# Kernel tuning notes

Measured on AMD Instinct MI355X. Metric: run time of the kernel, lower is better.

## Reference

```python
import jax, jax.numpy as jnp
import numpy as np

S_DIM, A_DIM, H_DIM = 256, 18, 256
E, NS, B = 5, 10, 4096  # ensemble, MC samples, batch


def setup_inputs() -> dict:
    key = jax.random.key(0)
    ks = iter(jax.random.split(key, 40))
    def kaiming(k, shape):
        return jax.random.normal(k, shape, jnp.float32) * np.float32(np.sqrt(2.0 / shape[-1]))
    inp = {
        "state": jax.random.normal(next(ks), (B, S_DIM), jnp.float32),
        "num_samples": NS,
    }
    dims = [(H_DIM, S_DIM), (H_DIM, H_DIM), (A_DIM, H_DIM)]
    for i, (o, ii) in enumerate(dims):
        inp[f"w_mu{i}"] = kaiming(next(ks), (E, o, ii))
        inp[f"w_rho{i}"] = jnp.full((E, o, ii), -3.0, jnp.float32)
        inp[f"b_mu{i}"] = jnp.zeros((E, o), jnp.float32)
        inp[f"b_rho{i}"] = jnp.full((E, o), -3.0, jnp.float32)
        inp[f"w_eps{i}"] = jax.random.normal(next(ks), (E, NS, o, ii), jnp.float32)
        inp[f"b_eps{i}"] = jax.random.normal(next(ks), (E, NS, o), jnp.float32)
    # uncertainty head: Linear(2A->H), ReLU, Linear(H->A), Softplus
    inp["uh_w1"] = kaiming(next(ks), (H_DIM, 2 * A_DIM))
    inp["uh_b1"] = jnp.zeros((H_DIM,), jnp.float32)
    inp["uh_w2"] = kaiming(next(ks), (A_DIM, H_DIM))
    inp["uh_b2"] = jnp.zeros((A_DIM,), jnp.float32)
    # risk head: Linear(3A->H), ReLU, Linear(H->1)
    inp["rh_w1"] = kaiming(next(ks), (H_DIM, 3 * A_DIM))
    inp["rh_b1"] = jnp.zeros((H_DIM,), jnp.float32)
    inp["rh_w2"] = kaiming(next(ks), (1, H_DIM))
    inp["rh_b2"] = jnp.zeros((1,), jnp.float32)
    return inp


def _kl(mu, sigma):
    # KL(N(mu, sigma) || N(0, 1)) summed over param dims -> per-ensemble [E]
    kl = -jnp.log(sigma) + (sigma ** 2 + mu ** 2) * 0.5 - 0.5
    return jnp.sum(kl, axis=tuple(range(1, mu.ndim)))


def _bayes(x, wmu, wrho, bmu, brho, weps, beps):
    # x: [E,S,B,in]; wmu: [E,out,in]; weps: [E,S,out,in]
    wsig = jax.nn.softplus(wrho)
    bsig = jax.nn.softplus(brho)
    w = wmu[:, None] + wsig[:, None] * weps        # [E,S,out,in]
    b = bmu[:, None] + bsig[:, None] * beps        # [E,S,out]
    y = jnp.einsum('esbi,esoi->esbo', x, w) + b[:, :, None, :]
    kl = _kl(wmu, wsig) + _kl(bmu, bsig)           # [E] (same for all MC samples)
    return y, kl


def reference(state, num_samples,
              w_mu0, w_rho0, b_mu0, b_rho0, w_eps0, b_eps0,
              w_mu1, w_rho1, b_mu1, b_rho1, w_eps1, b_eps1,
              w_mu2, w_rho2, b_mu2, b_rho2, w_eps2, b_eps2,
              uh_w1, uh_b1, uh_w2, uh_b2,
              rh_w1, rh_b1, rh_w2, rh_b2):
    e, ns = w_eps0.shape[0], w_eps0.shape[1]
    x = jnp.broadcast_to(state, (e, ns) + state.shape)          # [E,S,B,in]
    x, kl0 = _bayes(x, w_mu0, w_rho0, b_mu0, b_rho0, w_eps0, b_eps0)
    x = jax.nn.relu(x)  # dropout = identity (eval)
    x, kl1 = _bayes(x, w_mu1, w_rho1, b_mu1, b_rho1, w_eps1, b_eps1)
    x = jax.nn.relu(x)
    x, kl2 = _bayes(x, w_mu2, w_rho2, b_mu2, b_rho2, w_eps2, b_eps2)
    net_out = x.mean(axis=1)                                     # [E,B,A]
    q_mean = net_out.mean(axis=0)                                # [B,A]
    q_var = jnp.var(net_out, axis=0, ddof=1)                     # unbiased, as torch .var
    epistemic = q_var
    u_in = jnp.concatenate([q_mean, q_var], axis=-1)             # [B,2A]
    h = jax.nn.relu(u_in @ uh_w1.T + uh_b1)
    aleatoric = jax.nn.softplus(h @ uh_w2.T + uh_b2)             # [B,A]
    total_unc = epistemic + aleatoric
    r_in = jnp.concatenate([q_mean, epistemic, aleatoric], axis=-1)  # [B,3A]
    risk = jax.nn.relu(r_in @ rh_w1.T + rh_b1) @ rh_w2.T + rh_b2     # [B,1]
    s = 2.0 * jnp.sqrt(total_unc)
    lcb, ucb = q_mean - s, q_mean + s
    # total_kl = sum_e ns*kl_e ; divided by (E*num_samples) -> mean over ensemble
    kl_div = jnp.sum(kl0 + kl1 + kl2) / e
    return (q_mean, epistemic, aleatoric, total_unc, lcb, ucb, risk, kl_div)
```

## Files before the change

### kernel.cpp

```cpp
#include <hip/hip_runtime.h>
#include <hip/hip_bf16.h>


typedef __bf16 bf16x8 __attribute__((ext_vector_type(8)));
typedef float f32x4 __attribute__((ext_vector_type(4)));
typedef float f32x16 __attribute__((ext_vector_type(16)));
typedef unsigned short u16x4 __attribute__((ext_vector_type(4)));
typedef unsigned short u16x8 __attribute__((ext_vector_type(8)));

__device__ __forceinline__ unsigned short f2bf(float f) {
  unsigned int u = __builtin_bit_cast(unsigned int, f);
  u += 0x7fffu + ((u >> 16) & 1u);
  return (unsigned short)(u >> 16);
}

__device__ __forceinline__ float softplus_f(float x) {
  return (x > 20.f) ? x : __logf(1.f + __expf(x));
}

__device__ __forceinline__ float klterm(float m, float sg) {
  return -__logf(sg) + (sg * sg + m * m) * 0.5f - 0.5f;
}

__device__ __forceinline__ f32x16 mfma32(bf16x8 a, bf16x8 b, f32x16 c) {
  return __builtin_amdgcn_mfma_f32_32x32x16_bf16(a, b, c, 0, 0, 0);
}

template <int O>
__device__ __forceinline__ float wpanel_body(
    int p, int t, const float* __restrict__ wmu, const float* __restrict__ wrho,
    const float* __restrict__ weps, char* __restrict__ wf,
    char* __restrict__ lb) {
  int es = (O == 256) ? (p >> 3) : p;
  int osub = (O == 256) ? (p & 7) : 0;
  int e = es / 10, s = es - e * 10;
  float kl = 0.f;
  int i = (4 * t) & 255;
  int kt2 = i >> 4, byo = (i & 7) * 2, hi32 = 32 * ((i >> 3) & 1);
#pragma unroll
  for (int j = 0; j < 8; ++j) {
    int o = j * 4 + (t >> 6);
    int og = osub * 32 + o;
    float v[4];
    if (O == 256 || og < O) {
      size_t base = ((size_t)(e * O + og)) * 256 + i;
      f32x4 m4 = *(const f32x4*)(wmu + base);
      f32x4 r4 = *(const f32x4*)(wrho + base);
      f32x4 e4 = *(const f32x4*)(weps + ((size_t)((e * 10 + s) * O + og)) * 256 + i);
#pragma unroll
      for (int c = 0; c < 4; ++c) {
        float m = m4[c];
        float sg = softplus_f(r4[c]);
        v[c] = m + sg * e4[c];
        if (s == 0) kl += klterm(m, sg);
      }
    } else {
#pragma unroll
      for (int c = 0; c < 4; ++c) v[c] = 0.f;
    }
    u16x4 pk = {f2bf(v[0]), f2bf(v[1]), f2bf(v[2]), f2bf(v[3])};
    *(u16x4*)(lb + kt2 * 1024 + (o + hi32) * 16 + byo) = pk;
  }
  __syncthreads();
  char* dst = wf + (size_t)p * 16384;
#pragma unroll
  for (int j = 0; j < 4; ++j) {
    int idx = j * 256 + t;
    *(u16x8*)(dst + idx * 16) = *(const u16x8*)(lb + idx * 16);
  }
  return kl;
}

__device__ __forceinline__ void scvt_body(int gid, const float* __restrict__ s,
                                          unsigned short* __restrict__ d) {
  const f32x4* p = (const f32x4*)(s + (size_t)gid * 8);
  f32x4 x0 = p[0], x1 = p[1];
  u16x8 v = {f2bf(x0.x), f2bf(x0.y), f2bf(x0.z), f2bf(x0.w),
             f2bf(x1.x), f2bf(x1.y), f2bf(x1.z), f2bf(x1.w)};
  *(u16x8*)(d + (size_t)gid * 8) = v;
}

__global__ __launch_bounds__(256) void prep_kernel(
    const float* __restrict__ state, unsigned short* __restrict__ stateb,
    const float* __restrict__ wmu0, const float* __restrict__ wrho0,
    const float* __restrict__ weps0, char* __restrict__ W0f,
    const float* __restrict__ wmu1, const float* __restrict__ wrho1,
    const float* __restrict__ weps1, char* __restrict__ W1f,
    const float* __restrict__ wmu2, const float* __restrict__ wrho2,
    const float* __restrict__ weps2, char* __restrict__ W2f,
    const float* __restrict__ bmu0, const float* __restrict__ brho0,
    const float* __restrict__ beps0, const float* __restrict__ bmu1,
    const float* __restrict__ brho1, const float* __restrict__ beps1,
    const float* __restrict__ bmu2, const float* __restrict__ brho2,
    const float* __restrict__ beps2, float* __restrict__ bias0,
    float* __restrict__ bias1, float* __restrict__ bias2,
    float* __restrict__ partials) {
  __shared__ char lb[16384];
  int bid = blockIdx.x, t = threadIdx.x;
  float kl = 0.f;
  if (bid < 512) {
    scvt_body(bid * 256 + t, state, stateb);
  } else if (bid < 912) {
    kl = wpanel_body<256>(bid - 512, t, wmu0, wrho0, weps0, W0f, lb);
  } else if (bid < 1312) {
    kl = wpanel_body<256>(bid - 912, t, wmu1, wrho1, weps1, W1f, lb);
  } else if (bid < 1362) {
    kl = wpanel_body<18>(bid - 1312, t, wmu2, wrho2, weps2, W2f, lb);
  } else {
    int gid = (bid - 1362) * 256 + t;
    if (gid < 12800) {
      int es = gid >> 8, o = gid & 255, e = es / 10, s = es - e * 10;
      float m = bmu0[e * 256 + o];
      float sg = softplus_f(brho0[e * 256 + o]);
      bias0[gid] = m + sg * beps0[(e * 10 + s) * 256 + o];
      if (s == 0) kl = klterm(m, sg);
    } else if (gid < 25600) {
      int id = gid - 12800;
      int es = id >> 8, o = id & 255, e = es / 10, s = es - e * 10;
      float m = bmu1[e * 256 + o];
      float sg = softplus_f(brho1[e * 256 + o]);
      bias1[id] = m + sg * beps1[(e * 10 + s) * 256 + o];
      if (s == 0) kl = klterm(m, sg);
    } else if (gid < 27200) {
      int id = gid - 25600;
      int es = id >> 5, o = id & 31, e = es / 10, s = es - e * 10;
      if (o < 18) {
        float m = bmu2[e * 18 + o];
        float sg = softplus_f(brho2[e * 18 + o]);
        bias2[id] = m + sg * beps2[(e * 10 + s) * 18 + o];
        if (s == 0) kl = klterm(m, sg);
      } else {
        bias2[id] = 0.f;
      }
    }
  }
#pragma unroll
  for (int m = 32; m >= 1; m >>= 1) kl += __shfl_xor(kl, m);
  __shared__ float wsum[4];
  if ((t & 63) == 0) wsum[t >> 6] = kl;
  __syncthreads();
  if (t == 0) partials[bid] = wsum[0] + wsum[1] + wsum[2] + wsum[3];
}

__device__ __forceinline__ void mlp_layer32(const char* __restrict__ wA,
                                            const float* __restrict__ bias_es,
                                            int og, char* __restrict__ buf,
                                            int lane) {
  const char* a0p = wA + (size_t)(2 * og) * 16384;
  const char* a1p = a0p + 16384;
  const char* b0p = buf;
  const char* b1p = buf + 16384;
  int lo = lane * 16;
  f32x16 acc00, acc01, acc10, acc11;
#pragma unroll
  for (int c = 0; c < 16; ++c) {
    acc00[c] = 0.f; acc01[c] = 0.f; acc10[c] = 0.f; acc11[c] = 0.f;
  }

  bf16x8 a0c = *(const bf16x8*)(a0p + lo);
  bf16x8 a1c = *(const bf16x8*)(a1p + lo);
  bf16x8 b0c = *(const bf16x8*)(b0p + lo);
  bf16x8 b1c = *(const bf16x8*)(b1p + lo);
#pragma unroll
  for (int kp = 0; kp < 8; ++kp) {
    bf16x8 a0n = *(const bf16x8*)(a0p + (2 * kp + 1) * 1024 + lo);
    bf16x8 a1n = *(const bf16x8*)(a1p + (2 * kp + 1) * 1024 + lo);
    bf16x8 b0n = *(const bf16x8*)(b0p + (2 * kp + 1) * 1024 + lo);
    bf16x8 b1n = *(const bf16x8*)(b1p + (2 * kp + 1) * 1024 + lo);
    __builtin_amdgcn_s_setprio(1);
    acc00 = mfma32(a0c, b0c, acc00);
    acc01 = mfma32(a0c, b1c, acc01);
    acc10 = mfma32(a1c, b0c, acc10);
    acc11 = mfma32(a1c, b1c, acc11);
    __builtin_amdgcn_s_setprio(0);
    if (kp < 7) {
      a0c = *(const bf16x8*)(a0p + (2 * kp + 2) * 1024 + lo);
      a1c = *(const bf16x8*)(a1p + (2 * kp + 2) * 1024 + lo);
      b0c = *(const bf16x8*)(b0p + (2 * kp + 2) * 1024 + lo);
      b1c = *(const bf16x8*)(b1p + (2 * kp + 2) * 1024 + lo);
    }
    __builtin_amdgcn_s_setprio(1);
    acc00 = mfma32(a0n, b0n, acc00);
    acc01 = mfma32(a0n, b1n, acc01);
    acc10 = mfma32(a1n, b0n, acc10);
    acc11 = mfma32(a1n, b1n, acc11);
    __builtin_amdgcn_s_setprio(0);
  }
  __syncthreads();

  int hi = lane >> 5, bcol = lane & 31;
  auto epi = [&](const f32x16& A, int i, int j) {
    int obt = og * 64 + i * 32;
    char* fb = buf + (size_t)(j * 16) * 1024;
#pragma unroll
    for (int q = 0; q < 4; ++q) {
      int o0 = obt + 8 * q + 4 * hi;
      f32x4 bv = *(const f32x4*)(bias_es + o0);
      float v0 = fmaxf(A[4 * q + 0] + bv.x, 0.f);
      float v1 = fmaxf(A[4 * q + 1] + bv.y, 0.f);
      float v2 = fmaxf(A[4 * q + 2] + bv.z, 0.f);
      float v3 = fmaxf(A[4 * q + 3] + bv.w, 0.f);
      u16x4 pk = {f2bf(v0), f2bf(v1), f2bf(v2), f2bf(v3)};
      int kt2t = o0 >> 4;
      *(u16x4*)(fb + kt2t * 1024 + (bcol + 32 * (q & 1)) * 16 + 8 * hi) = pk;
    }
  };
  epi(acc00, 0, 0);
  epi(acc01, 0, 1);
  epi(acc10, 1, 0);
  epi(acc11, 1, 1);
  __syncthreads();
}

__global__ __launch_bounds__(256, 4) void mlp_fused(
    const unsigned short* __restrict__ stateb, const char* __restrict__ W0f,
    const char* __restrict__ W1f, const char* __restrict__ W2f,
    const float* __restrict__ bias0, const float* __restrict__ bias1,
    const float* __restrict__ bias2, float* __restrict__ y2) {
  __shared__ char buf[32768];
  int tid = threadIdx.x, w = tid >> 6, lane = tid & 63;
  int lo = lane * 16;

  int bid = blockIdx.x;
  int lin = (bid & 7) * 400 + (bid >> 3);
  int es = lin >> 6, b0 = (lin & 63) * 64;
  int og = w;

#pragma unroll
  for (int it = 0; it < 8; ++it) {
    int F = it * 4 + w, bt = F >> 4, kt2 = F & 15;
    const unsigned short* src =
        stateb + (size_t)(b0 + bt * 32 + (lane & 31)) * 256 + kt2 * 16 + (lane >> 5) * 8;
    *(u16x8*)(buf + F * 1024 + lo) = *(const u16x8*)src;
  }
  __syncthreads();

  mlp_layer32(W0f + (size_t)es * 131072, bias0 + es * 256, og, buf, lane);
  mlp_layer32(W1f + (size_t)es * 131072, bias1 + es * 256, og, buf, lane);

  if (w < 2) {
    int bt2 = w;
    f32x16 acc2;
#pragma unroll
    for (int c = 0; c < 16; ++c) acc2[c] = 0.f;
    const char* b2k = buf + (size_t)bt2 * 16384;
    const char* w2p = W2f + (size_t)es * 16384;
#pragma unroll
    for (int k = 0; k < 16; ++k) {
      bf16x8 a = *(const bf16x8*)(w2p + k * 1024 + lo);
      bf16x8 bb = *(const bf16x8*)(b2k + k * 1024 + lo);
      acc2 = mfma32(a, bb, acc2);
    }
    int hi = lane >> 5, bcol = lane & 31;
    int b_idx = b0 + bt2 * 32 + bcol;
    float* yp = y2 + ((size_t)es * 4096 + b_idx) * 20;
    float s[16];
#pragma unroll
    for (int q = 0; q < 4; ++q) {
      f32x4 bv = *(const f32x4*)(bias2 + es * 32 + 8 * q + 4 * hi);
      s[4 * q + 0] = acc2[4 * q + 0] + bv.x;
      s[4 * q + 1] = acc2[4 * q + 1] + bv.y;
      s[4 * q + 2] = acc2[4 * q + 2] + bv.z;
      s[4 * q + 3] = acc2[4 * q + 3] + bv.w;
    }
    if (hi == 0) {
      f32x4 v0 = {s[0], s[1], s[2], s[3]};
      f32x4 v1 = {s[4], s[5], s[6], s[7]};
      float2 v2 = {s[8], s[9]};
      *(f32x4*)(yp) = v0;
      *(f32x4*)(yp + 8) = v1;
      *(float2*)(yp + 16) = v2;
    } else {
      f32x4 v0 = {s[0], s[1], s[2], s[3]};
      f32x4 v1 = {s[4], s[5], s[6], s[7]};
      *(f32x4*)(yp + 4) = v0;
      *(f32x4*)(yp + 12) = v1;
    }
  }
}

__global__ __launch_bounds__(256) void heads_kernel(
    const float* __restrict__ y2, const float* __restrict__ partials,
    const float* __restrict__ uh_w1, const float* __restrict__ uh_b1,
    const float* __restrict__ uh_w2, const float* __restrict__ uh_b2,
    const float* __restrict__ rh_w1, const float* __restrict__ rh_b1,
    const float* __restrict__ rh_w2, const float* __restrict__ rh_b2,
    float* __restrict__ out) {
  int bid = blockIdx.x, t = threadIdx.x;
  if (bid == 512) {
    if (t < 64) {
      float acc = 0.f;
      for (int i = t; i < 1469; i += 64) acc += partials[i];
#pragma unroll
      for (int m = 32; m >= 1; m >>= 1) acc += __shfl_xor(acc, m);
      if (t == 0) out[446464] = acc * 0.2f;
    }
    return;
  }
  int b0 = bid * 8;

  __shared__ float ysh[8][1004];
  __shared__ float qsE[8][90];
  __shared__ float rin[8][56];
  __shared__ float h[8][260];

  for (int i = t; i < 2000; i += 256) {
    int r = i / 250, c = i - r * 250;
    int es_t = c / 5, part = c - es_t * 5;
    *(f32x4*)(&ysh[r][c * 4]) =
        *(const f32x4*)(y2 + ((size_t)es_t * 4096 + b0 + r) * 20 + part * 4);
  }
  __syncthreads();

  for (int i = t; i < 720; i += 256) {
    int r = i / 90, ae = i - r * 90;
    int a = ae / 5, e = ae - a * 5;
    float v = 0.f;
#pragma unroll
    for (int s = 0; s < 10; ++s) v += ysh[r][(e * 10 + s) * 20 + a];
    qsE[r][ae] = v * 0.1f;
  }
  __syncthreads();

  if (t < 144) {
    int r = t / 18, a = t - (t / 18) * 18;
    float qs = 0.f, qq = 0.f;
#pragma unroll
    for (int e = 0; e < 5; ++e) {
      float v = qsE[r][a * 5 + e];
      qs += v;
      qq += v * v;
    }
    float mean = qs * 0.2f;
    float var = fmaxf((qq - 5.f * mean * mean) * 0.25f, 0.f);
    rin[r][a] = mean;
    rin[r][18 + a] = var;
    out[(b0 + r) * 18 + a] = mean;
    out[73728 + (b0 + r) * 18 + a] = var;
  }
  __syncthreads();

  {
    f32x4 wv[9];
    const f32x4* wr = (const f32x4*)(uh_w1 + t * 36);
#pragma unroll
    for (int j = 0; j < 9; ++j) wv[j] = wr[j];
    float bb = uh_b1[t];
#pragma unroll
    for (int r = 0; r < 8; ++r) {
      float acc = bb;
#pragma unroll
      for (int j = 0; j < 9; ++j) {
        acc += wv[j].x * rin[r][j * 4] + wv[j].y * rin[r][j * 4 + 1] +
               wv[j].z * rin[r][j * 4 + 2] + wv[j].w * rin[r][j * 4 + 3];
      }
      h[r][t] = fmaxf(acc, 0.f);
    }
  }
  __syncthreads();

  if (t < 144) {
    int r = t / 18, a = t - (t / 18) * 18;
    float p = 0.f;
    const f32x4* w2r = (const f32x4*)(uh_w2 + a * 256);
#pragma unroll
    for (int j = 0; j < 64; ++j) {
      f32x4 wv = w2r[j];
      f32x4 hv = *(const f32x4*)(&h[r][j * 4]);
      p += wv.x * hv.x + wv.y * hv.y + wv.z * hv.z + wv.w * hv.w;
    }
    float alea = softplus_f(p + uh_b2[a]);
    float qm = rin[r][a], epi = rin[r][18 + a];
    float tu = epi + alea;
    float s2 = 2.f * sqrtf(tu);
    int b = b0 + r;
    out[2 * 73728 + b * 18 + a] = alea;
    out[3 * 73728 + b * 18 + a] = tu;
    out[4 * 73728 + b * 18 + a] = qm - s2;
    out[5 * 73728 + b * 18 + a] = qm + s2;
    rin[r][36 + a] = alea;
  }
  __syncthreads();

  {
    float w1v[54];
    const float2* wr2 = (const float2*)(rh_w1 + t * 54);
#pragma unroll
    for (int j = 0; j < 27; ++j) {
      float2 wv = wr2[j];
      w1v[j * 2] = wv.x;
      w1v[j * 2 + 1] = wv.y;
    }
    float bb = rh_b1[t];
#pragma unroll
    for (int r = 0; r < 8; ++r) {
      float acc = bb;
#pragma unroll
      for (int j = 0; j < 54; ++j) acc += w1v[j] * rin[r][j];
      h[r][t] = fmaxf(acc, 0.f);
    }
  }
  __syncthreads();

  if (t < 8) {
    float p = 0.f;
    const f32x4* w2r = (const f32x4*)(rh_w2);
#pragma unroll
    for (int j = 0; j < 64; ++j) {
      f32x4 wv = w2r[j];
      f32x4 hv = *(const f32x4*)(&h[t][j * 4]);
      p += wv.x * hv.x + wv.y * hv.y + wv.z * hv.z + wv.w * hv.w;
    }
    out[6 * 73728 + b0 + t] = p + rh_b2[0];
  }
}

extern "C" void kernel_launch(void* const* d_in, const int* in_sizes, int n_in,
                              void* d_out, int out_size, void* d_ws, size_t ws_size,
                              hipStream_t stream) {
  const float* state = (const float*)d_in[0];
  const float* w_mu0 = (const float*)d_in[2];
  const float* w_rho0 = (const float*)d_in[3];
  const float* b_mu0 = (const float*)d_in[4];
  const float* b_rho0 = (const float*)d_in[5];
  const float* w_eps0 = (const float*)d_in[6];
  const float* b_eps0 = (const float*)d_in[7];
  const float* w_mu1 = (const float*)d_in[8];
  const float* w_rho1 = (const float*)d_in[9];
  const float* b_mu1 = (const float*)d_in[10];
  const float* b_rho1 = (const float*)d_in[11];
  const float* w_eps1 = (const float*)d_in[12];
  const float* b_eps1 = (const float*)d_in[13];
  const float* w_mu2 = (const float*)d_in[14];
  const float* w_rho2 = (const float*)d_in[15];
  const float* b_mu2 = (const float*)d_in[16];
  const float* b_rho2 = (const float*)d_in[17];
  const float* w_eps2 = (const float*)d_in[18];
  const float* b_eps2 = (const float*)d_in[19];
  const float* uh_w1 = (const float*)d_in[20];
  const float* uh_b1 = (const float*)d_in[21];
  const float* uh_w2 = (const float*)d_in[22];
  const float* uh_b2 = (const float*)d_in[23];
  const float* rh_w1 = (const float*)d_in[24];
  const float* rh_b1 = (const float*)d_in[25];
  const float* rh_w2 = (const float*)d_in[26];
  const float* rh_b2 = (const float*)d_in[27];
  float* out = (float*)d_out;

  char* ws = (char*)d_ws;
  unsigned short* stateb = (unsigned short*)ws;
  char* W0f = ws + 2097152;
  char* W1f = W0f + 6553600;
  char* W2f = W1f + 6553600;
  float* bias0 = (float*)(W2f + 819200);
  float* bias1 = bias0 + 12800;
  float* bias2 = bias1 + 12800;
  float* y2 = bias2 + 1600;
  float* klpart = y2 + (size_t)50 * 4096 * 20;

  prep_kernel<<<1469, 256, 0, stream>>>(
      state, stateb, w_mu0, w_rho0, w_eps0, W0f, w_mu1, w_rho1, w_eps1, W1f,
      w_mu2, w_rho2, w_eps2, W2f, b_mu0, b_rho0, b_eps0, b_mu1, b_rho1, b_eps1,
      b_mu2, b_rho2, b_eps2, bias0, bias1, bias2, klpart);
  mlp_fused<<<3200, 256, 0, stream>>>(stateb, W0f, W1f, W2f, bias0, bias1,
                                      bias2, y2);
  heads_kernel<<<513, 256, 0, stream>>>(y2, klpart, uh_w1, uh_b1, uh_w2, uh_b2,
                                        rh_w1, rh_b1, rh_w2, rh_b2, out);
}
```

Measured before the change: 106.5 us.

## Double batch tile per block to 128 with 8 waves each owning 32 outputs

The fused MLP kernel now processes 128 batch rows per block with 512 threads instead of 64 rows with 256 threads. Each wave computes a 32-output by 128-batch strip, using one weight fragment against four activation fragments, rather than a 2x2 tile. The goal is to halve global weight traffic per batch row by reusing each ensemble/sample weight tile across more rows. The cost is a 64KB LDS activation buffer, more LDS reads per MFMA, and half as many blocks.

```diff
diff --git a/kernel.cpp b/kernel.cpp
--- a/kernel.cpp
+++ b/kernel.cpp
@@ -142,56 +142,56 @@
   if (t == 0) partials[bid] = wsum[0] + wsum[1] + wsum[2] + wsum[3];
 }
 
-__device__ __forceinline__ void mlp_layer32(const char* __restrict__ wA,
+__device__ __forceinline__ void mlp_layer1o(const char* __restrict__ wA,
                                             const float* __restrict__ bias_es,
-                                            int og, char* __restrict__ buf,
+                                            int w, char* __restrict__ buf,
                                             int lane) {
-  const char* a0p = wA + (size_t)(2 * og) * 16384;
-  const char* a1p = a0p + 16384;
-  const char* b0p = buf;
-  const char* b1p = buf + 16384;
+  const char* ap = wA + (size_t)w * 16384;
   int lo = lane * 16;
-  f32x16 acc00, acc01, acc10, acc11;
+  f32x16 acc0, acc1, acc2, acc3;
 #pragma unroll
   for (int c = 0; c < 16; ++c) {
-    acc00[c] = 0.f; acc01[c] = 0.f; acc10[c] = 0.f; acc11[c] = 0.f;
-  }
-
-  bf16x8 a0c = *(const bf16x8*)(a0p + lo);
-  bf16x8 a1c = *(const bf16x8*)(a1p + lo);
-  bf16x8 b0c = *(const bf16x8*)(b0p + lo);
-  bf16x8 b1c = *(const bf16x8*)(b1p + lo);
+    acc0[c] = 0.f; acc1[c] = 0.f; acc2[c] = 0.f; acc3[c] = 0.f;
+  }
+
+  bf16x8 ac = *(const bf16x8*)(ap + lo);
+  bf16x8 b0c = *(const bf16x8*)(buf + lo);
+  bf16x8 b1c = *(const bf16x8*)(buf + 16384 + lo);
+  bf16x8 b2c = *(const bf16x8*)(buf + 32768 + lo);
+  bf16x8 b3c = *(const bf16x8*)(buf + 49152 + lo);
 #pragma unroll
   for (int kp = 0; kp < 8; ++kp) {
-    bf16x8 a0n = *(const bf16x8*)(a0p + (2 * kp + 1) * 1024 + lo);
-    bf16x8 a1n = *(const bf16x8*)(a1p + (2 * kp + 1) * 1024 + lo);
-    bf16x8 b0n = *(const bf16x8*)(b0p + (2 * kp + 1) * 1024 + lo);
-    bf16x8 b1n = *(const bf16x8*)(b1p + (2 * kp + 1) * 1024 + lo);
+    bf16x8 an = *(const bf16x8*)(ap + (2 * kp + 1) * 1024 + lo);
+    bf16x8 b0n = *(const bf16x8*)(buf + (2 * kp + 1) * 1024 + lo);
+    bf16x8 b1n = *(const bf16x8*)(buf + 16384 + (2 * kp + 1) * 1024 + lo);
+    bf16x8 b2n = *(const bf16x8*)(buf + 32768 + (2 * kp + 1) * 1024 + lo);
+    bf16x8 b3n = *(const bf16x8*)(buf + 49152 + (2 * kp + 1) * 1024 + lo);
     __builtin_amdgcn_s_setprio(1);
-    acc00 = mfma32(a0c, b0c, acc00);
-    acc01 = mfma32(a0c, b1c, acc01);
-    acc10 = mfma32(a1c, b0c, acc10);
-    acc11 = mfma32(a1c, b1c, acc11);
+    acc0 = mfma32(ac, b0c, acc0);
+    acc1 = mfma32(ac, b1c, acc1);
+    acc2 = mfma32(ac, b2c, acc2);
+    acc3 = mfma32(ac, b3c, acc3);
     __builtin_amdgcn_s_setprio(0);
     if (kp < 7) {
-      a0c = *(const bf16x8*)(a0p + (2 * kp + 2) * 1024 + lo);
-      a1c = *(const bf16x8*)(a1p + (2 * kp + 2) * 1024 + lo);
-      b0c = *(const bf16x8*)(b0p + (2 * kp + 2) * 1024 + lo);
-      b1c = *(const bf16x8*)(b1p + (2 * kp + 2) * 1024 + lo);
+      ac = *(const bf16x8*)(ap + (2 * kp + 2) * 1024 + lo);
+      b0c = *(const bf16x8*)(buf + (2 * kp + 2) * 1024 + lo);
+      b1c = *(const bf16x8*)(buf + 16384 + (2 * kp + 2) * 1024 + lo);
+      b2c = *(const bf16x8*)(buf + 32768 + (2 * kp + 2) * 1024 + lo);
+      b3c = *(const bf16x8*)(buf + 49152 + (2 * kp + 2) * 1024 + lo);
     }
     __builtin_amdgcn_s_setprio(1);
-    acc00 = mfma32(a0n, b0n, acc00);
-    acc01 = mfma32(a0n, b1n, acc01);
-    acc10 = mfma32(a1n, b0n, acc10);
-    acc11 = mfma32(a1n, b1n, acc11);
+    acc0 = mfma32(an, b0n, acc0);
+    acc1 = mfma32(an, b1n, acc1);
+    acc2 = mfma32(an, b2n, acc2);
+    acc3 = mfma32(an, b3n, acc3);
     __builtin_amdgcn_s_setprio(0);
   }
   __syncthreads();
 
   int hi = lane >> 5, bcol = lane & 31;
-  auto epi = [&](const f32x16& A, int i, int j) {
-    int obt = og * 64 + i * 32;
-    char* fb = buf + (size_t)(j * 16) * 1024;
+  int obt = w * 32;
+  auto epi = [&](const f32x16& A, int bt) {
+    char* fb = buf + (size_t)(bt * 16) * 1024;
 #pragma unroll
     for (int q = 0; q < 4; ++q) {
       int o0 = obt + 8 * q + 4 * hi;
@@ -205,40 +205,39 @@
       *(u16x4*)(fb + kt2t * 1024 + (bcol + 32 * (q & 1)) * 16 + 8 * hi) = pk;
     }
   };
-  epi(acc00, 0, 0);
-  epi(acc01, 0, 1);
-  epi(acc10, 1, 0);
-  epi(acc11, 1, 1);
-  __syncthreads();
-}
-
-__global__ __launch_bounds__(256, 4) void mlp_fused(
+  epi(acc0, 0);
+  epi(acc1, 1);
+  epi(acc2, 2);
+  epi(acc3, 3);
+  __syncthreads();
+}
+
+__global__ __launch_bounds__(512, 4) void mlp_fused(
     const unsigned short* __restrict__ stateb, const char* __restrict__ W0f,
     const char* __restrict__ W1f, const char* __restrict__ W2f,
     const float* __restrict__ bias0, const float* __restrict__ bias1,
     const float* __restrict__ bias2, float* __restrict__ y2) {
-  __shared__ char buf[32768];
+  __shared__ char buf[65536];
   int tid = threadIdx.x, w = tid >> 6, lane = tid & 63;
   int lo = lane * 16;
 
   int bid = blockIdx.x;
-  int lin = (bid & 7) * 400 + (bid >> 3);
-  int es = lin >> 6, b0 = (lin & 63) * 64;
-  int og = w;
+  int lin = (bid & 7) * 200 + (bid >> 3);
+  int es = lin >> 5, b0 = (lin & 31) * 128;
 
 #pragma unroll
   for (int it = 0; it < 8; ++it) {
-    int F = it * 4 + w, bt = F >> 4, kt2 = F & 15;
+    int F = it * 8 + w, bt = F >> 4, kt2 = F & 15;
     const unsigned short* src =
         stateb + (size_t)(b0 + bt * 32 + (lane & 31)) * 256 + kt2 * 16 + (lane >> 5) * 8;
     *(u16x8*)(buf + F * 1024 + lo) = *(const u16x8*)src;
   }
   __syncthreads();
 
-  mlp_layer32(W0f + (size_t)es * 131072, bias0 + es * 256, og, buf, lane);
-  mlp_layer32(W1f + (size_t)es * 131072, bias1 + es * 256, og, buf, lane);
-
-  if (w < 2) {
+  mlp_layer1o(W0f + (size_t)es * 131072, bias0 + es * 256, w, buf, lane);
+  mlp_layer1o(W1f + (size_t)es * 131072, bias1 + es * 256, w, buf, lane);
+
+  if (w < 4) {
     int bt2 = w;
     f32x16 acc2;
 #pragma unroll
@@ -462,7 +461,7 @@
       state, stateb, w_mu0, w_rho0, w_eps0, W0f, w_mu1, w_rho1, w_eps1, W1f,
       w_mu2, w_rho2, w_eps2, W2f, b_mu0, b_rho0, b_eps0, b_mu1, b_rho1, b_eps1,
       b_mu2, b_rho2, b_eps2, bias0, bias1, bias2, klpart);
-  mlp_fused<<<3200, 256, 0, stream>>>(stateb, W0f, W1f, W2f, bias0, bias1,
+  mlp_fused<<<1600, 512, 0, stream>>>(stateb, W0f, W1f, W2f, bias0, bias1,
                                       bias2, y2);
   heads_kernel<<<513, 256, 0, stream>>>(y2, klpart, uh_w1, uh_b1, uh_w2, uh_b2,
                                         rh_w1, rh_b1, rh_w2, rh_b2, out);
```

Result: slower. 108.9 us (+2.3%).
